# Optimization experiments

Hardware: AMD Instinct MI355X
Metric: run time of the kernel (lower is better)

Reference implementation:

```python
import jax, jax.numpy as jnp
import numpy as np
import math

B, S, H = 2, 2048, 2048
NH, NKV, HD = 16, 4, 128


def _rope_tables(seq_len, head_dim):
    # Standard RoPE: freqs over half dim, duplicated to full head_dim.
    inv_freq = 1.0 / (10000.0 ** (np.arange(0, head_dim, 2, dtype=np.float32) / head_dim))
    t = np.arange(seq_len, dtype=np.float32)
    freqs = np.outer(t, inv_freq)  # [S, HD/2]
    emb = np.concatenate([freqs, freqs], axis=-1)  # [S, HD]
    return jnp.asarray(np.cos(emb)), jnp.asarray(np.sin(emb))


def setup_inputs() -> dict:
    key = jax.random.key(0)
    k1, k2, k3, k4 = jax.random.split(key, 4)
    cos, sin = _rope_tables(S, HD)
    return {
        "x": jax.random.normal(k1, (B, S, H), dtype=jnp.float32),
        "cos": cos,
        "sin": sin,
        "Wq": jax.random.normal(k2, (H, NH * HD), dtype=jnp.float32) * (1.0 / math.sqrt(H)),
        "Wkv": jax.random.normal(k3, (H, 2 * NKV * HD), dtype=jnp.float32) * (1.0 / math.sqrt(H)),
        "Wo": jax.random.normal(k4, (NH * HD, H), dtype=jnp.float32) * (1.0 / math.sqrt(NH * HD)),
    }


def _rotate_half(x):
    x1, x2 = jnp.split(x, 2, axis=-1)
    return jnp.concatenate([-x2, x1], axis=-1)


def _apply_rotary(x, cos, sin):
    # x: [B, S, nheads, HD]; cos/sin: [S, HD]
    c = cos[None, :, None, :]
    s = sin[None, :, None, :]
    return x * c + _rotate_half(x) * s


def reference(x, cos, sin, Wq, Wkv, Wo):
    b, s, _ = x.shape
    q = (x @ Wq).reshape(b, s, NH, HD)
    kv = x @ Wkv
    k, v = jnp.split(kv, [NKV * HD], axis=-1)
    k = k.reshape(b, s, NKV, HD)
    v = v.reshape(b, s, NKV, HD)
    q = _apply_rotary(q, cos, sin)
    k = _apply_rotary(k, cos, sin)
    # to [B, heads, S, HD]
    q = jnp.transpose(q, (0, 2, 1, 3))
    k = jnp.transpose(k, (0, 2, 1, 3))
    v = jnp.transpose(v, (0, 2, 1, 3))
    # GQA: repeat K/V heads
    rep = NH // NKV
    k = jnp.repeat(k, rep, axis=1)
    v = jnp.repeat(v, rep, axis=1)
    scale = jnp.asarray(1.0 / math.sqrt(HD), dtype=x.dtype)
    scores = jnp.einsum('bhqd,bhkd->bhqk', q * scale, k)  # [B, NH, S, S]
    causal = jnp.tril(jnp.ones((s, s), dtype=jnp.bool_))
    scores = jnp.where(causal, scores, jnp.asarray(-jnp.inf, scores.dtype))
    attn = jax.nn.softmax(scores, axis=-1)
    out = jnp.einsum('bhqk,bhkd->bhqd', attn, v)
    out = jnp.transpose(out, (0, 2, 1, 3)).reshape(b, s, NH * HD)
    return out @ Wo
```

## Files before the change

### kernel.cpp

```cpp
#include <hip/hip_runtime.h>
#include <math.h>

#define NB 2
#define SEQ 2048
#define HDIM 2048
#define NHD 16
#define NKVH 4
#define HEADD 128
#define MROWS (NB*SEQ)
#define NQCOLS (NHD*HEADD)
#define QKVCOLS 3072

typedef unsigned short ushortT;
typedef __attribute__((ext_vector_type(8))) short short8;
typedef __attribute__((ext_vector_type(4))) float floatx4;
typedef __attribute__((ext_vector_type(4))) unsigned short ushort4v;

__device__ __forceinline__ ushortT f2bf(float f) {
  union { float f; unsigned int u; } v; v.f = f;
  unsigned int r = v.u + 0x7FFFu + ((v.u >> 16) & 1u);
  return (ushortT)(r >> 16);
}
__device__ __forceinline__ float bf2f(ushortT u) {
  union { unsigned int u; float f; } v; v.u = ((unsigned int)u) << 16;
  return v.f;
}

__device__ __forceinline__ void gload16(const ushortT* g, ushortT* l) {
  __builtin_amdgcn_global_load_lds(
      (const __attribute__((address_space(1))) void*)g,
      (__attribute__((address_space(3))) void*)l, 16, 0, 0);
}

__global__ __launch_bounds__(256) void cast_bf16_kernel(
    const float* __restrict__ in, ushortT* __restrict__ out, int n4) {
  int i = blockIdx.x * 256 + threadIdx.x;
  if (i >= n4) return;
  float4 v = ((const float4*)in)[i];
  ushort4v o;
  o.x = f2bf(v.x); o.y = f2bf(v.y); o.z = f2bf(v.z); o.w = f2bf(v.w);
  ((ushort4v*)out)[i] = o;
}

__global__ __launch_bounds__(256) void transpose_cast_kernel(
    const float* __restrict__ in, ushortT* __restrict__ out, int R, int C) {
  __shared__ ushortT tile[32][33];
  int c0 = blockIdx.x * 32, r0 = blockIdx.y * 32;
  int tx = threadIdx.x & 31, ty = threadIdx.x >> 5;
#pragma unroll
  for (int i = 0; i < 4; ++i)
    tile[ty + i*8][tx] = f2bf(in[(size_t)(r0 + ty + i*8) * C + c0 + tx]);
  __syncthreads();
#pragma unroll
  for (int i = 0; i < 4; ++i)
    out[(size_t)(c0 + ty + i*8) * R + r0 + tx] = tile[tx][ty + i*8];
}

__global__ __launch_bounds__(256) void gemm_bt_kernel(
    const ushortT* __restrict__ A, const ushortT* __restrict__ Bt,
    void* __restrict__ C, int M, int N, int K, int c_fp32) {
  __shared__ __align__(16) ushortT lA[128 * 64];
  __shared__ __align__(16) ushortT lB[128 * 64];
  const int m0 = blockIdx.y * 128;
  const int n0 = blockIdx.x * 128;
  const int tid = threadIdx.x;
  const int wave = tid >> 6, lane = tid & 63;
  const int g = lane >> 4, l15 = lane & 15;
  const int wm = (wave >> 1) * 64, wn = (wave & 1) * 64;
  const int sw = l15 & 7;

  floatx4 acc[4][4] = {};

  for (int kt = 0; kt < K; kt += 64) {
    __syncthreads();
#pragma unroll
    for (int i = 0; i < 4; ++i) {
      int s = i * 256 + tid;
      int r = s >> 3, j = s & 7;
      int col8 = j ^ (r & 7);
      gload16(A  + (size_t)(m0 + r) * K + kt + col8 * 8, lA + s * 8);
      gload16(Bt + (size_t)(n0 + r) * K + kt + col8 * 8, lB + s * 8);
    }
    __syncthreads();
#pragma unroll
    for (int ks = 0; ks < 2; ++ks) {
      short8 af[4], bfv[4];
#pragma unroll
      for (int t = 0; t < 4; ++t) {
        af[t]  = *(const short8*)(lA + (wm + t * 16 + l15) * 64 + ((ks * 4 + g) ^ sw) * 8);
        bfv[t] = *(const short8*)(lB + (wn + t * 16 + l15) * 64 + ((ks * 4 + g) ^ sw) * 8);
      }
#pragma unroll
      for (int mt = 0; mt < 4; ++mt)
#pragma unroll
        for (int nt = 0; nt < 4; ++nt)
          acc[mt][nt] = __builtin_amdgcn_mfma_f32_16x16x32_bf16(
              af[mt], bfv[nt], acc[mt][nt], 0, 0, 0);
    }
  }

#pragma unroll
  for (int mt = 0; mt < 4; ++mt)
#pragma unroll
    for (int nt = 0; nt < 4; ++nt)
#pragma unroll
      for (int r = 0; r < 4; ++r) {
        int row = m0 + wm + mt * 16 + g * 4 + r;
        int col = n0 + wn + nt * 16 + l15;
        float v = acc[mt][nt][r];
        if (c_fp32) ((float*)C)[(size_t)row * N + col] = v;
        else ((ushortT*)C)[(size_t)row * N + col] = f2bf(v);
      }
}

__global__ __launch_bounds__(256) void rope_q_kernel(
    const ushortT* __restrict__ QKVtmp, const float* __restrict__ cosT,
    const float* __restrict__ sinT, ushortT* __restrict__ Qr) {
  int idx = blockIdx.x * 256 + threadIdx.x;
  int d = idx & 63;
  int t = idx >> 6;
  int h = t & (NHD - 1);
  int bs = t >> 4;
  int s = bs & (SEQ - 1);
  int b = bs >> 11;
  float c = cosT[s * HEADD + d], sn = sinT[s * HEADD + d];
  float q1 = bf2f(QKVtmp[(size_t)bs * QKVCOLS + h * HEADD + d]);
  float q2 = bf2f(QKVtmp[(size_t)bs * QKVCOLS + h * HEADD + d + 64]);
  size_t o = ((size_t)(b * NHD + h) * SEQ + s) * HEADD + d;
  Qr[o]      = f2bf(q1 * c - q2 * sn);
  Qr[o + 64] = f2bf(q2 * c + q1 * sn);
}

__global__ __launch_bounds__(256) void rope_k_kernel(
    const ushortT* __restrict__ QKVtmp, const float* __restrict__ cosT,
    const float* __restrict__ sinT, ushortT* __restrict__ Kr) {
  int idx = blockIdx.x * 256 + threadIdx.x;
  int d = idx & 63;
  int t = idx >> 6;
  int kvh = t & (NKVH - 1);
  int bs = t >> 2;
  int s = bs & (SEQ - 1);
  int b = bs >> 11;
  float c = cosT[s * HEADD + d], sn = sinT[s * HEADD + d];
  float k1 = bf2f(QKVtmp[(size_t)bs * QKVCOLS + 2048 + kvh * HEADD + d]);
  float k2 = bf2f(QKVtmp[(size_t)bs * QKVCOLS + 2048 + kvh * HEADD + d + 64]);
  size_t o = ((size_t)(b * NKVH + kvh) * SEQ + s) * HEADD + d;
  Kr[o]      = f2bf(k1 * c - k2 * sn);
  Kr[o + 64] = f2bf(k2 * c + k1 * sn);
}

__global__ __launch_bounds__(256) void v_relayout_kernel(
    const ushortT* __restrict__ QKVtmp, ushortT* __restrict__ Vt) {
  __shared__ ushortT tile[32][33];
  int bk = blockIdx.z;
  int b = bk >> 2, kvh = bk & 3;
  int s0 = blockIdx.x * 32, d0 = blockIdx.y * 32;
  int tx = threadIdx.x & 31, ty = threadIdx.x >> 5;
#pragma unroll
  for (int i = 0; i < 4; ++i) {
    int s = s0 + ty + i * 8;
    tile[ty + i * 8][tx] =
        QKVtmp[(size_t)(b * SEQ + s) * QKVCOLS + 2560 + kvh * HEADD + d0 + tx];
  }
  __syncthreads();
#pragma unroll
  for (int i = 0; i < 4; ++i) {
    int d = d0 + ty + i * 8;
    Vt[((size_t)bk * HEADD + d) * SEQ + s0 + tx] = tile[tx][ty + i * 8];
  }
}

__global__ __launch_bounds__(256) void attn_kernel(
    const ushortT* __restrict__ Q,
    const ushortT* __restrict__ Kg,
    const ushortT* __restrict__ Vg,
    ushortT* __restrict__ Oa) {
  __shared__ __align__(16) ushortT lK[64 * 128];
  __shared__ __align__(16) ushortT lV[128 * 64];
  __shared__ __align__(16) ushortT lP[4 * 16 * 72];

  const int tid = threadIdx.x;
  const int w = tid >> 6, lane = tid & 63;
  const int g = lane >> 4, l15 = lane & 15;
  const int sw = l15 & 7;
  const int bh = blockIdx.x;
  const int b = bh >> 4, h = bh & 15;
  const int kvh = h >> 2;
  const int qi = 31 - (int)blockIdx.y;
  const int q0 = qi << 6;
  const int qw = q0 + w * 16;

  const float SC = 0.08838834764831845f * 1.4426950408889634f;

  short8 qf[4];
  {
    const ushortT* qp =
        Q + (((size_t)(b * NHD + h)) * SEQ + qw + l15) * HEADD + g * 8;
#pragma unroll
    for (int ks = 0; ks < 4; ++ks) qf[ks] = *(const short8*)(qp + ks * 32);
  }

  floatx4 o[8] = {};
  float m_s = -INFINITY;
  float l_s = 0.f;

  const ushortT* kbase = Kg + ((size_t)(b * NKVH + kvh)) * SEQ * HEADD;
  const ushortT* vbase = Vg + ((size_t)(b * NKVH + kvh)) * HEADD * SEQ;
  ushortT* pw = lP + w * 16 * 72;

  const int nkt = qi + 1;
  for (int kt = 0; kt < nkt; ++kt) {
    __syncthreads();
#pragma unroll
    for (int ii = 0; ii < 4; ++ii) {
      int s = ii * 256 + tid;
      int r = s >> 4, j = (s & 15) ^ (r & 7);
      gload16(kbase + (size_t)(kt * 64 + r) * HEADD + j * 8, lK + s * 8);
    }
#pragma unroll
    for (int ii = 0; ii < 4; ++ii) {
      int s = ii * 256 + tid;
      int r = s >> 3, j = (s & 7) ^ (r & 7);
      gload16(vbase + (size_t)r * SEQ + kt * 64 + j * 8, lV + s * 8);
    }
    __syncthreads();

    const int rel = qw - kt * 64;

    floatx4 sc[4] = {};
    __builtin_amdgcn_s_setprio(1);
#pragma unroll
    for (int nt = 0; nt < 4; ++nt) {
      if (nt * 16 > rel + 15) continue;
#pragma unroll
      for (int ks = 0; ks < 4; ++ks) {
        short8 kf = *(const short8*)(lK + (nt * 16 + l15) * 128 + ((ks * 4 + g) ^ sw) * 8);
        sc[nt] = __builtin_amdgcn_mfma_f32_16x16x32_bf16(kf, qf[ks], sc[nt], 0, 0, 0);
      }
    }
    __builtin_amdgcn_s_setprio(0);

    const bool needmask = (kt * 64 + 63) > qw;
    float ps[4][4];
    float mx = -INFINITY;
#pragma unroll
    for (int nt = 0; nt < 4; ++nt)
#pragma unroll
      for (int r = 0; r < 4; ++r) {
        float v = sc[nt][r] * SC;
        if (needmask) {
          int kg = kt * 64 + nt * 16 + g * 4 + r;
          if (kg > qw + l15) v = -INFINITY;
        }
        ps[nt][r] = v;
        mx = fmaxf(mx, v);
      }
    mx = fmaxf(mx, __shfl_xor(mx, 16));
    mx = fmaxf(mx, __shfl_xor(mx, 32));
    float mn = fmaxf(m_s, mx);
    float alpha = __builtin_amdgcn_exp2f(m_s - mn);
    m_s = mn;
    float rs = 0.f;
#pragma unroll
    for (int nt = 0; nt < 4; ++nt) {
      ushort4v pk;
#pragma unroll
      for (int r = 0; r < 4; ++r) {
        float e = __builtin_amdgcn_exp2f(ps[nt][r] - mn);
        rs += e;
        ((ushortT*)&pk)[r] = f2bf(e);
      }
      *(ushort4v*)(pw + l15 * 72 + nt * 16 + g * 4) = pk;
    }
    rs += __shfl_xor(rs, 16);
    rs += __shfl_xor(rs, 32);
    l_s = l_s * alpha + rs;
#pragma unroll
    for (int dt = 0; dt < 8; ++dt)
#pragma unroll
      for (int r = 0; r < 4; ++r) o[dt][r] *= alpha;

    __builtin_amdgcn_s_setprio(1);
#pragma unroll
    for (int ks = 0; ks < 2; ++ks) {
      if (kt * 64 + ks * 32 > qw + 15) continue;
      short8 bp = *(const short8*)(pw + l15 * 72 + ks * 32 + g * 8);
#pragma unroll
      for (int dt = 0; dt < 8; ++dt) {
        short8 vf = *(const short8*)(lV + (dt * 16 + l15) * 64 + ((ks * 4 + g) ^ sw) * 8);
        o[dt] = __builtin_amdgcn_mfma_f32_16x16x32_bf16(vf, bp, o[dt], 0, 0, 0);
      }
    }
    __builtin_amdgcn_s_setprio(0);
  }

  {
    float inv = 1.f / l_s;
    int qg = qw + l15;
#pragma unroll
    for (int dt = 0; dt < 8; ++dt) {
      ushort4v ov;
#pragma unroll
      for (int r = 0; r < 4; ++r) ((ushortT*)&ov)[r] = f2bf(o[dt][r] * inv);
      *(ushort4v*)(Oa + (size_t)(b * SEQ + qg) * NQCOLS + h * HEADD + dt * 16 + g * 4) = ov;
    }
  }
}

extern "C" void kernel_launch(void* const* d_in, const int* in_sizes, int n_in,
                              void* d_out, int out_size, void* d_ws, size_t ws_size,
                              hipStream_t stream) {
  const float* x    = (const float*)d_in[0];
  const float* cosT = (const float*)d_in[1];
  const float* sinT = (const float*)d_in[2];
  const float* Wq   = (const float*)d_in[3];
  const float* Wkv  = (const float*)d_in[4];
  const float* Wo   = (const float*)d_in[5];

  char* ws = (char*)d_ws;
  ushortT* x_bf   = (ushortT*)(ws + 0);
  ushortT* Wqkvt  = (ushortT*)(ws + 16777216);
  ushortT* Wot    = (ushortT*)(ws + 29360128);
  ushortT* QKVtmp = (ushortT*)(ws + 37748736);
  ushortT* Qr     = (ushortT*)(ws + 62914560);
  ushortT* Kr     = (ushortT*)(ws + 79691776);
  ushortT* Vt     = (ushortT*)(ws + 83886080);
  ushortT* Oattn  = QKVtmp;

  cast_bf16_kernel<<<8192, 256, 0, stream>>>(x, x_bf, (MROWS * HDIM) / 4);
  transpose_cast_kernel<<<dim3(64, 64), 256, 0, stream>>>(Wq, Wqkvt, HDIM, NQCOLS);
  transpose_cast_kernel<<<dim3(32, 64), 256, 0, stream>>>(Wkv, Wqkvt + 2048 * 2048, HDIM, 1024);
  transpose_cast_kernel<<<dim3(64, 64), 256, 0, stream>>>(Wo, Wot, NQCOLS, HDIM);

  gemm_bt_kernel<<<dim3(24, 32), 256, 0, stream>>>(x_bf, Wqkvt, QKVtmp, MROWS, QKVCOLS, HDIM, 0);

  rope_q_kernel<<<16384, 256, 0, stream>>>(QKVtmp, cosT, sinT, Qr);
  rope_k_kernel<<<4096, 256, 0, stream>>>(QKVtmp, cosT, sinT, Kr);
  v_relayout_kernel<<<dim3(64, 4, 8), 256, 0, stream>>>(QKVtmp, Vt);

  attn_kernel<<<dim3(32, 32), 256, 0, stream>>>(Qr, Kr, Vt, Oattn);

  gemm_bt_kernel<<<dim3(16, 32), 256, 0, stream>>>(Oattn, Wot, d_out, MROWS, HDIM, NQCOLS, 1);
}
```

Baseline: 337.4 us.

## Skip softmax rescale under max threshold, use packed bf16 convert, XOR-swizzle P buffer

The online softmax now keeps the running max and skips rescaling the accumulator when the new tile max stays within a threshold of the old one (checked wave-wide). The scale is folded into an FMA inside exp2. A hardware packed bf16 conversion instruction replaces manual rounding. The P scratch buffer drops its padding and uses an XOR swizzle to avoid LDS bank conflicts. The lazy rescale removes most of the 32-register multiply per tile, but lets exponentials grow up to 2^8, which slightly raises the risk of bf16 precision loss.

```diff
diff --git a/kernel.cpp b/kernel.cpp
--- a/kernel.cpp
+++ b/kernel.cpp
@@ -24,6 +24,12 @@
 __device__ __forceinline__ float bf2f(ushortT u) {
   union { unsigned int u; float f; } v; v.u = ((unsigned int)u) << 16;
   return v.f;
+}
+
+__device__ __forceinline__ unsigned int cvt_pk_bf16(float lo, float hi) {
+  unsigned int r;
+  asm("v_cvt_pk_bf16_f32 %0, %1, %2" : "=v"(r) : "v"(lo), "v"(hi));
+  return r;
 }
 
 __device__ __forceinline__ void gload16(const ushortT* g, ushortT* l) {
@@ -177,7 +183,7 @@
     ushortT* __restrict__ Oa) {
   __shared__ __align__(16) ushortT lK[64 * 128];
   __shared__ __align__(16) ushortT lV[128 * 64];
-  __shared__ __align__(16) ushortT lP[4 * 16 * 72];
+  __shared__ __align__(16) ushortT lP[4 * 16 * 64];
 
   const int tid = threadIdx.x;
   const int w = tid >> 6, lane = tid & 63;
@@ -191,6 +197,7 @@
   const int qw = q0 + w * 16;
 
   const float SC = 0.08838834764831845f * 1.4426950408889634f;
+  const float THR = 8.0f / SC;
 
   short8 qf[4];
   {
@@ -206,7 +213,7 @@
 
   const ushortT* kbase = Kg + ((size_t)(b * NKVH + kvh)) * SEQ * HEADD;
   const ushortT* vbase = Vg + ((size_t)(b * NKVH + kvh)) * HEADD * SEQ;
-  ushortT* pw = lP + w * 16 * 72;
+  ushortT* pw = lP + w * 16 * 64;
 
   const int nkt = qi + 1;
   for (int kt = 0; kt < nkt; ++kt) {
@@ -247,7 +254,7 @@
     for (int nt = 0; nt < 4; ++nt)
 #pragma unroll
       for (int r = 0; r < 4; ++r) {
-        float v = sc[nt][r] * SC;
+        float v = sc[nt][r];
         if (needmask) {
           int kg = kt * 64 + nt * 16 + g * 4 + r;
           if (kg > qw + l15) v = -INFINITY;
@@ -257,34 +264,45 @@
       }
     mx = fmaxf(mx, __shfl_xor(mx, 16));
     mx = fmaxf(mx, __shfl_xor(mx, 32));
-    float mn = fmaxf(m_s, mx);
-    float alpha = __builtin_amdgcn_exp2f(m_s - mn);
-    m_s = mn;
+
+    float mn;
+    if (__all(mx <= m_s + THR)) {
+      mn = m_s;
+    } else {
+      mn = fmaxf(m_s, mx);
+      float alpha = __builtin_amdgcn_exp2f((m_s - mn) * SC);
+      l_s *= alpha;
+#pragma unroll
+      for (int dt = 0; dt < 8; ++dt)
+#pragma unroll
+        for (int r = 0; r < 4; ++r) o[dt][r] *= alpha;
+      m_s = mn;
+    }
+    const float mnSC = mn * SC;
+
     float rs = 0.f;
 #pragma unroll
     for (int nt = 0; nt < 4; ++nt) {
-      ushort4v pk;
+      float e[4];
 #pragma unroll
       for (int r = 0; r < 4; ++r) {
-        float e = __builtin_amdgcn_exp2f(ps[nt][r] - mn);
-        rs += e;
-        ((ushortT*)&pk)[r] = f2bf(e);
-      }
-      *(ushort4v*)(pw + l15 * 72 + nt * 16 + g * 4) = pk;
+        e[r] = __builtin_amdgcn_exp2f(__builtin_fmaf(ps[nt][r], SC, -mnSC));
+        rs += e[r];
+      }
+      uint2 pk;
+      pk.x = cvt_pk_bf16(e[0], e[1]);
+      pk.y = cvt_pk_bf16(e[2], e[3]);
+      *(uint2*)(pw + l15 * 64 + (((nt * 2 + (g >> 1)) ^ sw) * 8 + (g & 1) * 4)) = pk;
     }
     rs += __shfl_xor(rs, 16);
     rs += __shfl_xor(rs, 32);
-    l_s = l_s * alpha + rs;
-#pragma unroll
-    for (int dt = 0; dt < 8; ++dt)
-#pragma unroll
-      for (int r = 0; r < 4; ++r) o[dt][r] *= alpha;
+    l_s += rs;
 
     __builtin_amdgcn_s_setprio(1);
 #pragma unroll
     for (int ks = 0; ks < 2; ++ks) {
       if (kt * 64 + ks * 32 > qw + 15) continue;
-      short8 bp = *(const short8*)(pw + l15 * 72 + ks * 32 + g * 8);
+      short8 bp = *(const short8*)(pw + l15 * 64 + ((ks * 4 + g) ^ sw) * 8);
 #pragma unroll
       for (int dt = 0; dt < 8; ++dt) {
         short8 vf = *(const short8*)(lV + (dt * 16 + l15) * 64 + ((ks * 4 + g) ^ sw) * 8);
@@ -299,10 +317,10 @@
     int qg = qw + l15;
 #pragma unroll
     for (int dt = 0; dt < 8; ++dt) {
-      ushort4v ov;
-#pragma unroll
-      for (int r = 0; r < 4; ++r) ((ushortT*)&ov)[r] = f2bf(o[dt][r] * inv);
-      *(ushort4v*)(Oa + (size_t)(b * SEQ + qg) * NQCOLS + h * HEADD + dt * 16 + g * 4) = ov;
+      uint2 ov;
+      ov.x = cvt_pk_bf16(o[dt][0] * inv, o[dt][1] * inv);
+      ov.y = cvt_pk_bf16(o[dt][2] * inv, o[dt][3] * inv);
+      *(uint2*)(Oa + (size_t)(b * SEQ + qg) * NQCOLS + h * HEADD + dt * 16 + g * 4) = ov;
     }
   }
 }
```

Measured after the change: 339.2 us. No clear change (+0.5%).
